# Kernel tuning notes

Hardware: AMD Instinct MI355X
Metric: run time of the kernel (lower is better)

Reference implementation:

```python
import jax, jax.numpy as jnp
import numpy as np


def setup_inputs() -> dict:
    key = jax.random.key(0)
    ks = jax.random.split(key, 8)
    B, H, W, C = 4, 64, 64, 64
    d = C // 8
    x = jax.random.normal(ks[0], (B, H, W, C), dtype=jnp.float32)
    # 1x1 conv kernels (spectral-normalized in the original; here we use the
    # already-normalized weight matrices directly, scaled to unit-ish norm)
    Wf = jax.random.normal(ks[1], (C, d), dtype=jnp.float32) * (1.0 / np.sqrt(C))
    bf = jnp.zeros((d,), dtype=jnp.float32)
    Wg = jax.random.normal(ks[2], (C, d), dtype=jnp.float32) * (1.0 / np.sqrt(C))
    bg = jnp.zeros((d,), dtype=jnp.float32)
    Wh = jax.random.normal(ks[3], (C, C), dtype=jnp.float32) * (1.0 / np.sqrt(C))
    bh = jnp.zeros((C,), dtype=jnp.float32)
    gamma = jnp.float32(1.0)
    return {"x": x, "Wf": Wf, "bf": bf, "Wg": Wg, "bg": bg,
            "Wh": Wh, "bh": bh, "gamma": gamma}


def reference(x, Wf, bf, Wg, bg, Wh, bh, gamma):
    # x: [B, H, W, C] (NHWC, as Keras Conv2D default)
    B, H, W, C = x.shape
    N = H * W
    # 1x1 convs == per-pixel channel matmuls
    q = jnp.einsum('bhwc,cd->bhwd', x, Wf) + bf   # [B,H,W,C//8]
    k = jnp.einsum('bhwc,cd->bhwd', x, Wg) + bg   # [B,H,W,C//8]
    v = jnp.einsum('bhwc,cd->bhwd', x, Wh) + bh   # [B,H,W,C]
    q = q.reshape(B, N, -1)
    k = k.reshape(B, N, -1)
    v = v.reshape(B, N, C)
    # full non-causal attention (no 1/sqrt(d) scaling in the original)
    s = jnp.einsum('bnd,bmd->bnm', q, k)          # [B,N,N]
    s = jax.nn.softmax(s, axis=-1)
    o = jnp.einsum('bnm,bmc->bnc', s, v)          # [B,N,C]
    o = o.reshape(B, H, W, C)
    return gamma * o + x
```

## Files before the change

kernel.cpp:

```cpp
#include <hip/hip_runtime.h>
#include <hip/hip_bf16.h>

#define BATCH 4
#define NTOK 4096
#define CCH 64
#define KSPLIT 4
#define KPB (NTOK / KSPLIT)
#define NTILE (KPB / 64)

typedef short s16x8 __attribute__((ext_vector_type(8)));
typedef float f32x4 __attribute__((ext_vector_type(4)));

static __device__ __forceinline__ unsigned short f2bf(float f) {
    union { __hip_bfloat16 h; unsigned short u; } cv;
    cv.h = __float2bfloat16(f);
    return cv.u;
}
static __device__ __forceinline__ float bf2f(unsigned short u) {
    union { unsigned int u; float f; } c; c.u = ((unsigned)u) << 16;
    return c.f;
}
static __device__ __forceinline__ float bf_split(float f, unsigned short& h) {
    h = f2bf(f);
    return f - bf2f(h);
}
static __device__ __forceinline__ unsigned pack_trunc(float a, float b) {
    union { float f; unsigned u; } ca, cb; ca.f = a; cb.f = b;
    return (ca.u >> 16) | (cb.u & 0xFFFF0000u);
}

__global__ __launch_bounds__(256) void proj_kernel(
    const float* __restrict__ xg,
    const float* __restrict__ Wf, const float* __restrict__ bf_,
    const float* __restrict__ Wg, const float* __restrict__ bg,
    const float* __restrict__ Wh, const float* __restrict__ bh,
    unsigned short* __restrict__ Qp, unsigned short* __restrict__ Kp,
    unsigned short* __restrict__ vTg)
{
    __shared__ float xS[32 * 68];
    __shared__ float WfT[8 * 68];
    __shared__ float WgT[8 * 68];
    __shared__ unsigned short vtS[64 * 40];

    const int t = threadIdx.x;
    const int b = blockIdx.x >> 7;
    const int n0 = (blockIdx.x & 127) * 32;

    const float* xrow = xg + ((size_t)b * NTOK + n0) * CCH;
    for (int f = t; f < 512; f += 256) {
        int r = f >> 4, c4 = (f & 15) * 4;
        *(float4*)(xS + r * 68 + c4) = *(const float4*)(xrow + r * 64 + c4);
    }
    for (int e = t; e < 512; e += 256) {
        int ci = e >> 3, j = e & 7;
        WfT[j * 68 + ci] = Wf[e];
        WgT[j * 68 + ci] = Wg[e];
    }
    __syncthreads();

    const int w = t >> 6, lane = t & 63, ml = lane & 15, quad = lane >> 4;

    {
        s16x8 a0, a1;
        #pragma unroll
        for (int j = 0; j < 8; ++j) {
            a0[j] = (short)f2bf(Wh[(quad * 8 + j) * 64 + w * 16 + ml]);
            a1[j] = (short)f2bf(Wh[(32 + quad * 8 + j) * 64 + w * 16 + ml]);
        }
        #pragma unroll
        for (int nf = 0; nf < 2; ++nf) {
            int tok = nf * 16 + ml;
            float4 r0 = *(const float4*)(xS + tok * 68 + quad * 8);
            float4 r1 = *(const float4*)(xS + tok * 68 + quad * 8 + 4);
            float4 r2 = *(const float4*)(xS + tok * 68 + 32 + quad * 8);
            float4 r3 = *(const float4*)(xS + tok * 68 + 32 + quad * 8 + 4);
            s16x8 b0, b1;
            b0[0] = (short)f2bf(r0.x); b0[1] = (short)f2bf(r0.y);
            b0[2] = (short)f2bf(r0.z); b0[3] = (short)f2bf(r0.w);
            b0[4] = (short)f2bf(r1.x); b0[5] = (short)f2bf(r1.y);
            b0[6] = (short)f2bf(r1.z); b0[7] = (short)f2bf(r1.w);
            b1[0] = (short)f2bf(r2.x); b1[1] = (short)f2bf(r2.y);
            b1[2] = (short)f2bf(r2.z); b1[3] = (short)f2bf(r2.w);
            b1[4] = (short)f2bf(r3.x); b1[5] = (short)f2bf(r3.y);
            b1[6] = (short)f2bf(r3.z); b1[7] = (short)f2bf(r3.w);
            f32x4 cc = __builtin_amdgcn_mfma_f32_16x16x32_bf16(a0, b0, (f32x4){0.f,0.f,0.f,0.f}, 0, 0, 0);
            cc = __builtin_amdgcn_mfma_f32_16x16x32_bf16(a1, b1, cc, 0, 0, 0);
            #pragma unroll
            for (int reg = 0; reg < 4; ++reg) {
                int cout = w * 16 + quad * 4 + reg;
                vtS[cout * 40 + nf * 16 + ml] = f2bf(cc[reg] + bh[cout]);
            }
        }
    }

    {
        int r = t >> 3, j = t & 7;
        float q = bf_[j], k = bg[j];
        for (int ci = 0; ci < 64; ci += 4) {
            float4 x4 = *(const float4*)(xS + r * 68 + ci);
            float4 wf4 = *(const float4*)(WfT + j * 68 + ci);
            float4 wg4 = *(const float4*)(WgT + j * 68 + ci);
            q += x4.x * wf4.x + x4.y * wf4.y + x4.z * wf4.z + x4.w * wf4.w;
            k += x4.x * wg4.x + x4.y * wg4.y + x4.z * wg4.z + x4.w * wg4.w;
        }
        unsigned short qh, kh;
        float qres = bf_split(q, qh);
        float kres = bf_split(k, kh);
        unsigned short ql = f2bf(qres), kl = f2bf(kres);
        size_t base = ((size_t)b * NTOK + n0 + r) * 32;
        Qp[base + j]      = qh;
        Qp[base + 8 + j]  = ql;
        Qp[base + 16 + j] = qh;
        Qp[base + 24 + j] = 0;
        Kp[base + j]      = kh;
        Kp[base + 8 + j]  = kh;
        Kp[base + 16 + j] = kl;
        Kp[base + 24 + j] = 0;
    }
    __syncthreads();

    {
        int c_ = t >> 2, chunk = t & 3;
        uint4 v = *(const uint4*)(vtS + c_ * 40 + chunk * 8);
        *(uint4*)(vTg + ((size_t)b * CCH + c_) * NTOK + n0 + chunk * 8) = v;
    }
}

__global__ __launch_bounds__(256, 4) void attn_kernel(
    const unsigned short* __restrict__ Qp,
    const unsigned short* __restrict__ Kp,
    const unsigned short* __restrict__ vTg,
    unsigned short* __restrict__ Opart,
    float* __restrict__ lpart)
{
    __shared__ unsigned short PS[2][64 * 72];

    const int t = threadIdx.x;
    const int blk = blockIdx.x;
    const int b = blk >> 8;
    const int qt = (blk >> 2) & 63;
    const int ks = blk & 3;
    const int m0 = qt * 64;
    const int kb0 = ks * KPB;
    const int w = t >> 6, lane = t & 63;
    const int ml = lane & 15, quad = lane >> 4;

    const unsigned short* qpb = Qp + (size_t)b * NTOK * 32;
    const unsigned short* kpb = Kp + (size_t)b * NTOK * 32;
    const unsigned short* vtb = vTg + (size_t)b * CCH * NTOK;

    s16x8 qf[4];
    #pragma unroll
    for (int g = 0; g < 4; ++g)
        qf[g] = *(const s16x8*)(qpb + (size_t)(m0 + g * 16 + ml) * 32 + quad * 8);

    s16x8 ones;
    #pragma unroll
    for (int i = 0; i < 8; ++i) ones[i] = (short)0x3F80;

    f32x4 o[4], l[4];
    #pragma unroll
    for (int g = 0; g < 4; ++g) { o[g] = (f32x4){0.f,0.f,0.f,0.f}; l[g] = (f32x4){0.f,0.f,0.f,0.f}; }
    const f32x4 zz = {0.f, 0.f, 0.f, 0.f};

    s16x8 kf = *(const s16x8*)(kpb + (size_t)(kb0 + w * 16 + ml) * 32 + quad * 8);

    for (int jt = 0; jt < NTILE; ++jt) {
        const int buf = jt & 1;
        const int kb = kb0 + jt * 64;

        f32x4 sg[4];
        #pragma unroll
        for (int g = 0; g < 4; ++g)
            sg[g] = __builtin_amdgcn_mfma_f32_16x16x32_bf16(kf, qf[g], zz, 0, 0, 0);

        {
            int kbn = kb0 + ((jt + 1) & (NTILE - 1)) * 64;
            kf = *(const s16x8*)(kpb + (size_t)(kbn + w * 16 + ml) * 32 + quad * 8);
        }
        s16x8 vf0 = *(const s16x8*)(vtb + (size_t)(w * 16 + ml) * NTOK + kb + quad * 8);
        s16x8 vf1 = *(const s16x8*)(vtb + (size_t)(w * 16 + ml) * NTOK + kb + 32 + quad * 8);

        #pragma unroll
        for (int g = 0; g < 4; ++g) {
            float p0 = exp2f(fmaf(sg[g][0], 1.442695041f, -28.85390082f));
            float p1 = exp2f(fmaf(sg[g][1], 1.442695041f, -28.85390082f));
            float p2 = exp2f(fmaf(sg[g][2], 1.442695041f, -28.85390082f));
            float p3 = exp2f(fmaf(sg[g][3], 1.442695041f, -28.85390082f));
            uint2 d = { pack_trunc(p0, p1), pack_trunc(p2, p3) };
            *(uint2*)(&PS[buf][(g * 16 + ml) * 72 + w * 16 + quad * 4]) = d;
        }
        __syncthreads();

        #pragma unroll
        for (int g = 0; g < 4; ++g) {
            s16x8 ap0 = *(const s16x8*)(&PS[buf][(g * 16 + ml) * 72 + quad * 8]);
            s16x8 ap1 = *(const s16x8*)(&PS[buf][(g * 16 + ml) * 72 + 32 + quad * 8]);
            l[g] = __builtin_amdgcn_mfma_f32_16x16x32_bf16(ap0, ones, l[g], 0, 0, 0);
            l[g] = __builtin_amdgcn_mfma_f32_16x16x32_bf16(ap1, ones, l[g], 0, 0, 0);
            o[g] = __builtin_amdgcn_mfma_f32_16x16x32_bf16(ap0, vf0, o[g], 0, 0, 0);
            o[g] = __builtin_amdgcn_mfma_f32_16x16x32_bf16(ap1, vf1, o[g], 0, 0, 0);
        }
    }

    const size_t obase = (size_t)ks * (BATCH * NTOK * 64)
                       + (size_t)b * NTOK * 64;
    #pragma unroll
    for (int g = 0; g < 4; ++g)
        #pragma unroll
        for (int reg = 0; reg < 4; ++reg) {
            int q = m0 + g * 16 + quad * 4 + reg;
            Opart[obase + (size_t)q * 64 + w * 16 + ml] = f2bf(o[g][reg]);
        }
    if (w == 0 && ml == 0) {
        #pragma unroll
        for (int g = 0; g < 4; ++g)
            #pragma unroll
            for (int reg = 0; reg < 4; ++reg)
                lpart[ks * (BATCH * NTOK) + b * NTOK + m0 + g * 16 + quad * 4 + reg] = l[g][reg];
    }
}

__global__ __launch_bounds__(256) void combine_kernel(
    const float* __restrict__ xg,
    const unsigned short* __restrict__ Opart,
    const float* __restrict__ lpart,
    const float* __restrict__ gammaPtr,
    float* __restrict__ out)
{
    const int i4 = blockIdx.x * 256 + threadIdx.x;
    const int base = i4 * 4;
    const int tok = base >> 6;

    float lsum = 0.f;
    #pragma unroll
    for (int s = 0; s < KSPLIT; ++s)
        lsum += lpart[s * (BATCH * NTOK) + tok];

    float o0 = 0.f, o1 = 0.f, o2 = 0.f, o3 = 0.f;
    #pragma unroll
    for (int s = 0; s < KSPLIT; ++s) {
        uint2 u = *(const uint2*)(Opart + (size_t)s * (BATCH * NTOK * 64) + base);
        o0 += bf2f((unsigned short)(u.x & 0xFFFF));
        o1 += bf2f((unsigned short)(u.x >> 16));
        o2 += bf2f((unsigned short)(u.y & 0xFFFF));
        o3 += bf2f((unsigned short)(u.y >> 16));
    }
    const float4 x4 = *(const float4*)(xg + base);
    const float gi = gammaPtr[0] / lsum;
    float4 r;
    r.x = gi * o0 + x4.x;
    r.y = gi * o1 + x4.y;
    r.z = gi * o2 + x4.z;
    r.w = gi * o3 + x4.w;
    *(float4*)(out + base) = r;
}

extern "C" void kernel_launch(void* const* d_in, const int* in_sizes, int n_in,
                              void* d_out, int out_size, void* d_ws, size_t ws_size,
                              hipStream_t stream) {
    const float* x  = (const float*)d_in[0];
    const float* Wf = (const float*)d_in[1];
    const float* bf = (const float*)d_in[2];
    const float* Wg = (const float*)d_in[3];
    const float* bg = (const float*)d_in[4];
    const float* Wh = (const float*)d_in[5];
    const float* bh = (const float*)d_in[6];
    const float* gamma = (const float*)d_in[7];
    float* out = (float*)d_out;

    char* ws = (char*)d_ws;
    unsigned short* Qp    = (unsigned short*)ws;
    unsigned short* Kp    = (unsigned short*)(ws + (1u << 20));
    unsigned short* vTg   = (unsigned short*)(ws + (2u << 20));
    unsigned short* Opart = (unsigned short*)(ws + (4u << 20));
    float*          lpart = (float*)(ws + (12u << 20));

    proj_kernel<<<BATCH * 128, 256, 0, stream>>>(x, Wf, bf, Wg, bg, Wh, bh,
                                                 Qp, Kp, vTg);
    attn_kernel<<<BATCH * 64 * KSPLIT, 256, 0, stream>>>(Qp, Kp, vTg, Opart, lpart);
    combine_kernel<<<(BATCH * NTOK * CCH) / 1024, 256, 0, stream>>>(x, Opart, lpart, gamma, out);
}
```

Measured before the change: 109.3 us.

## Keep P in registers, stage K/V tiles in LDS, coalesce output writes

Restructures the attention loop so each wave owns 16 query rows and computes S transposed (keys×queries). The exponentiated P then feeds the PV MFMA directly as the B operand, with no round trip through shared memory. K and V tiles are cooperatively loaded into double-buffered LDS, with global prefetch of the next tile overlapped with the exp work. The output is transposed through LDS for vectorized coalesced stores. This removes the per-tile P write/read and the redundant per-wave global V loads. In exchange it adds LDS traffic for K/V and a key-index permutation that must match the MFMA layout.

```diff
diff --git a/kernel.cpp b/kernel.cpp
--- a/kernel.cpp
+++ b/kernel.cpp
@@ -27,6 +27,9 @@
 static __device__ __forceinline__ unsigned pack_trunc(float a, float b) {
     union { float f; unsigned u; } ca, cb; ca.f = a; cb.f = b;
     return (ca.u >> 16) | (cb.u & 0xFFFF0000u);
+}
+static __device__ __forceinline__ unsigned pack_rne(float a, float b) {
+    return ((unsigned)f2bf(b) << 16) | f2bf(a);
 }
 
 __global__ __launch_bounds__(256) void proj_kernel(
@@ -133,7 +136,8 @@
     unsigned short* __restrict__ Opart,
     float* __restrict__ lpart)
 {
-    __shared__ unsigned short PS[2][64 * 72];
+    __shared__ unsigned short VS[2][64 * 72];
+    __shared__ unsigned short KS[2][64 * 36];
 
     const int t = threadIdx.x;
     const int blk = blockIdx.x;
@@ -149,75 +153,111 @@
     const unsigned short* kpb = Kp + (size_t)b * NTOK * 32;
     const unsigned short* vtb = vTg + (size_t)b * CCH * NTOK;
 
-    s16x8 qf[4];
-    #pragma unroll
-    for (int g = 0; g < 4; ++g)
-        qf[g] = *(const s16x8*)(qpb + (size_t)(m0 + g * 16 + ml) * 32 + quad * 8);
+    const s16x8 qf = *(const s16x8*)(qpb + (size_t)(m0 + w * 16 + ml) * 32 + quad * 8);
+
+    const int keyA = 8 * (ml >> 2) + (ml & 3);
 
     s16x8 ones;
     #pragma unroll
     for (int i = 0; i < 8; ++i) ones[i] = (short)0x3F80;
 
-    f32x4 o[4], l[4];
-    #pragma unroll
-    for (int g = 0; g < 4; ++g) { o[g] = (f32x4){0.f,0.f,0.f,0.f}; l[g] = (f32x4){0.f,0.f,0.f,0.f}; }
+    f32x4 o[4];
+    #pragma unroll
+    for (int cg = 0; cg < 4; ++cg) o[cg] = (f32x4){0.f, 0.f, 0.f, 0.f};
+    f32x4 lac = {0.f, 0.f, 0.f, 0.f};
     const f32x4 zz = {0.f, 0.f, 0.f, 0.f};
 
-    s16x8 kf = *(const s16x8*)(kpb + (size_t)(kb0 + w * 16 + ml) * 32 + quad * 8);
+    const int vrow = t >> 2, vcb = (t & 3) * 2;
+    const int krow = t >> 2, kpart = t & 3;
+
+    {
+        uint4 va = *(const uint4*)(vtb + (size_t)vrow * NTOK + kb0 + vcb * 8);
+        uint4 vb = *(const uint4*)(vtb + (size_t)vrow * NTOK + kb0 + (vcb + 1) * 8);
+        uint4 kk = *(const uint4*)(kpb + (size_t)(kb0 + krow) * 32 + kpart * 8);
+        *(uint4*)(&VS[0][vrow * 72 + vcb * 8]) = va;
+        *(uint4*)(&VS[0][vrow * 72 + (vcb + 1) * 8]) = vb;
+        *(uint4*)(&KS[0][krow * 36 + kpart * 8]) = kk;
+    }
 
     for (int jt = 0; jt < NTILE; ++jt) {
         const int buf = jt & 1;
-        const int kb = kb0 + jt * 64;
-
-        f32x4 sg[4];
+        __syncthreads();
+
+        const unsigned short* ksb = &KS[buf][0];
+        s16x8 kf0 = *(const s16x8*)(ksb + (keyA) * 36 + quad * 8);
+        s16x8 kf1 = *(const s16x8*)(ksb + (keyA + 4) * 36 + quad * 8);
+        s16x8 kf2 = *(const s16x8*)(ksb + (32 + keyA) * 36 + quad * 8);
+        s16x8 kf3 = *(const s16x8*)(ksb + (32 + keyA + 4) * 36 + quad * 8);
+
+        f32x4 sA0 = __builtin_amdgcn_mfma_f32_16x16x32_bf16(kf0, qf, zz, 0, 0, 0);
+        f32x4 sB0 = __builtin_amdgcn_mfma_f32_16x16x32_bf16(kf1, qf, zz, 0, 0, 0);
+        f32x4 sA1 = __builtin_amdgcn_mfma_f32_16x16x32_bf16(kf2, qf, zz, 0, 0, 0);
+        f32x4 sB1 = __builtin_amdgcn_mfma_f32_16x16x32_bf16(kf3, qf, zz, 0, 0, 0);
+
+        uint4 va, vb, kk;
+        const bool more = (jt + 1 < NTILE);
+        if (more) {
+            const int kbn = kb0 + (jt + 1) * 64;
+            va = *(const uint4*)(vtb + (size_t)vrow * NTOK + kbn + vcb * 8);
+            vb = *(const uint4*)(vtb + (size_t)vrow * NTOK + kbn + (vcb + 1) * 8);
+            kk = *(const uint4*)(kpb + (size_t)(kbn + krow) * 32 + kpart * 8);
+        }
+
+        union { unsigned u[4]; s16x8 h; } bf0, bf1;
+        bf0.u[0] = pack_trunc(exp2f(fmaf(sA0[0], 1.442695041f, -28.85390082f)),
+                              exp2f(fmaf(sA0[1], 1.442695041f, -28.85390082f)));
+        bf0.u[1] = pack_trunc(exp2f(fmaf(sA0[2], 1.442695041f, -28.85390082f)),
+                              exp2f(fmaf(sA0[3], 1.442695041f, -28.85390082f)));
+        bf0.u[2] = pack_trunc(exp2f(fmaf(sB0[0], 1.442695041f, -28.85390082f)),
+                              exp2f(fmaf(sB0[1], 1.442695041f, -28.85390082f)));
+        bf0.u[3] = pack_trunc(exp2f(fmaf(sB0[2], 1.442695041f, -28.85390082f)),
+                              exp2f(fmaf(sB0[3], 1.442695041f, -28.85390082f)));
+        bf1.u[0] = pack_trunc(exp2f(fmaf(sA1[0], 1.442695041f, -28.85390082f)),
+                              exp2f(fmaf(sA1[1], 1.442695041f, -28.85390082f)));
+        bf1.u[1] = pack_trunc(exp2f(fmaf(sA1[2], 1.442695041f, -28.85390082f)),
+                              exp2f(fmaf(sA1[3], 1.442695041f, -28.85390082f)));
+        bf1.u[2] = pack_trunc(exp2f(fmaf(sB1[0], 1.442695041f, -28.85390082f)),
+                              exp2f(fmaf(sB1[1], 1.442695041f, -28.85390082f)));
+        bf1.u[3] = pack_trunc(exp2f(fmaf(sB1[2], 1.442695041f, -28.85390082f)),
+                              exp2f(fmaf(sB1[3], 1.442695041f, -28.85390082f)));
+
+        if (more) {
+            *(uint4*)(&VS[buf ^ 1][vrow * 72 + vcb * 8]) = va;
+            *(uint4*)(&VS[buf ^ 1][vrow * 72 + (vcb + 1) * 8]) = vb;
+            *(uint4*)(&KS[buf ^ 1][krow * 36 + kpart * 8]) = kk;
+        }
+
+        lac = __builtin_amdgcn_mfma_f32_16x16x32_bf16(ones, bf0.h, lac, 0, 0, 0);
+        lac = __builtin_amdgcn_mfma_f32_16x16x32_bf16(ones, bf1.h, lac, 0, 0, 0);
+
+        const unsigned short* vs = &VS[buf][0];
         #pragma unroll
-        for (int g = 0; g < 4; ++g)
-            sg[g] = __builtin_amdgcn_mfma_f32_16x16x32_bf16(kf, qf[g], zz, 0, 0, 0);
-
-        {
-            int kbn = kb0 + ((jt + 1) & (NTILE - 1)) * 64;
-            kf = *(const s16x8*)(kpb + (size_t)(kbn + w * 16 + ml) * 32 + quad * 8);
-        }
-        s16x8 vf0 = *(const s16x8*)(vtb + (size_t)(w * 16 + ml) * NTOK + kb + quad * 8);
-        s16x8 vf1 = *(const s16x8*)(vtb + (size_t)(w * 16 + ml) * NTOK + kb + 32 + quad * 8);
-
-        #pragma unroll
-        for (int g = 0; g < 4; ++g) {
-            float p0 = exp2f(fmaf(sg[g][0], 1.442695041f, -28.85390082f));
-            float p1 = exp2f(fmaf(sg[g][1], 1.442695041f, -28.85390082f));
-            float p2 = exp2f(fmaf(sg[g][2], 1.442695041f, -28.85390082f));
-            float p3 = exp2f(fmaf(sg[g][3], 1.442695041f, -28.85390082f));
-            uint2 d = { pack_trunc(p0, p1), pack_trunc(p2, p3) };
-            *(uint2*)(&PS[buf][(g * 16 + ml) * 72 + w * 16 + quad * 4]) = d;
-        }
-        __syncthreads();
-
-        #pragma unroll
-        for (int g = 0; g < 4; ++g) {
-            s16x8 ap0 = *(const s16x8*)(&PS[buf][(g * 16 + ml) * 72 + quad * 8]);
-            s16x8 ap1 = *(const s16x8*)(&PS[buf][(g * 16 + ml) * 72 + 32 + quad * 8]);
-            l[g] = __builtin_amdgcn_mfma_f32_16x16x32_bf16(ap0, ones, l[g], 0, 0, 0);
-            l[g] = __builtin_amdgcn_mfma_f32_16x16x32_bf16(ap1, ones, l[g], 0, 0, 0);
-            o[g] = __builtin_amdgcn_mfma_f32_16x16x32_bf16(ap0, vf0, o[g], 0, 0, 0);
-            o[g] = __builtin_amdgcn_mfma_f32_16x16x32_bf16(ap1, vf1, o[g], 0, 0, 0);
-        }
-    }
-
-    const size_t obase = (size_t)ks * (BATCH * NTOK * 64)
-                       + (size_t)b * NTOK * 64;
-    #pragma unroll
-    for (int g = 0; g < 4; ++g)
-        #pragma unroll
-        for (int reg = 0; reg < 4; ++reg) {
-            int q = m0 + g * 16 + quad * 4 + reg;
-            Opart[obase + (size_t)q * 64 + w * 16 + ml] = f2bf(o[g][reg]);
-        }
-    if (w == 0 && ml == 0) {
-        #pragma unroll
-        for (int g = 0; g < 4; ++g)
-            #pragma unroll
-            for (int reg = 0; reg < 4; ++reg)
-                lpart[ks * (BATCH * NTOK) + b * NTOK + m0 + g * 16 + quad * 4 + reg] = l[g][reg];
+        for (int cg = 0; cg < 4; ++cg) {
+            s16x8 vA0 = *(const s16x8*)(vs + (cg * 16 + ml) * 72 + quad * 8);
+            s16x8 vA1 = *(const s16x8*)(vs + (cg * 16 + ml) * 72 + 32 + quad * 8);
+            o[cg] = __builtin_amdgcn_mfma_f32_16x16x32_bf16(vA0, bf0.h, o[cg], 0, 0, 0);
+            o[cg] = __builtin_amdgcn_mfma_f32_16x16x32_bf16(vA1, bf1.h, o[cg], 0, 0, 0);
+        }
+    }
+
+    if (quad == 0)
+        lpart[ks * (BATCH * NTOK) + b * NTOK + m0 + w * 16 + ml] = lac[0];
+
+    __syncthreads();
+    unsigned short* TR = &VS[0][0];
+    #pragma unroll
+    for (int cg = 0; cg < 4; ++cg) {
+        uint2 dd = { pack_rne(o[cg][0], o[cg][1]), pack_rne(o[cg][2], o[cg][3]) };
+        *(uint2*)(&TR[(w * 16 + ml) * 72 + cg * 16 + quad * 4]) = dd;
+    }
+    __syncthreads();
+    {
+        int ql = t >> 2, ch = t & 3;
+        uint4 u0 = *(const uint4*)(&TR[ql * 72 + ch * 16]);
+        uint4 u1 = *(const uint4*)(&TR[ql * 72 + ch * 16 + 8]);
+        size_t obase = ((size_t)ks * (BATCH * NTOK) + (size_t)b * NTOK + m0 + ql) * 64;
+        *(uint4*)(Opart + obase + ch * 16) = u0;
+        *(uint4*)(Opart + obase + ch * 16 + 8) = u1;
     }
 }
 
```

Measured after the change: 126.0 us. 15.3% more time.

## Restructure attention so each wave owns key tiles with register-resident P

Applied to the files above, without the earlier changes.

The attention kernel drops the shared-memory P exchange and the per-tile block barrier. Each wave now processes its own subset of key tiles for all 64 queries and all 64 channels, keeping P in registers as the MFMA B operand. Per-wave partial outputs and row sums are reduced through LDS at the end. The key split drops from 4 to 2, K is compacted to 16 halves and staged once in LDS, and proj_kernel converts x to bf16 once in shared memory. In exchange the kernel holds many more accumulator registers (occupancy bound lowered to 2 blocks per SIMD), runs fewer blocks, and adds a serialized end-of-kernel reduction.

```diff
diff --git a/kernel.cpp b/kernel.cpp
--- a/kernel.cpp
+++ b/kernel.cpp
@@ -4,12 +4,16 @@
 #define BATCH 4
 #define NTOK 4096
 #define CCH 64
-#define KSPLIT 4
+#define KSPLIT 2
 #define KPB (NTOK / KSPLIT)
 #define NTILE (KPB / 64)
+#define TPW (NTILE / 4)
 
 typedef short s16x8 __attribute__((ext_vector_type(8)));
 typedef float f32x4 __attribute__((ext_vector_type(4)));
+
+#define LOG2E 1.442695041f
+#define ESHIFT (-28.85390082f)
 
 static __device__ __forceinline__ unsigned short f2bf(float f) {
     union { __hip_bfloat16 h; unsigned short u; } cv;
@@ -27,6 +31,12 @@
 static __device__ __forceinline__ unsigned pack_trunc(float a, float b) {
     union { float f; unsigned u; } ca, cb; ca.f = a; cb.f = b;
     return (ca.u >> 16) | (cb.u & 0xFFFF0000u);
+}
+static __device__ __forceinline__ unsigned pack_rne(float a, float b) {
+    return ((unsigned)f2bf(b) << 16) | f2bf(a);
+}
+static __device__ __forceinline__ float pexp(float s) {
+    return exp2f(fmaf(s, LOG2E, ESHIFT));
 }
 
 __global__ __launch_bounds__(256) void proj_kernel(
@@ -38,6 +48,7 @@
     unsigned short* __restrict__ vTg)
 {
     __shared__ float xS[32 * 68];
+    __shared__ unsigned short xbS[32 * 72];
     __shared__ float WfT[8 * 68];
     __shared__ float WgT[8 * 68];
     __shared__ unsigned short vtS[64 * 40];
@@ -49,7 +60,10 @@
     const float* xrow = xg + ((size_t)b * NTOK + n0) * CCH;
     for (int f = t; f < 512; f += 256) {
         int r = f >> 4, c4 = (f & 15) * 4;
-        *(float4*)(xS + r * 68 + c4) = *(const float4*)(xrow + r * 64 + c4);
+        float4 v = *(const float4*)(xrow + r * 64 + c4);
+        *(float4*)(xS + r * 68 + c4) = v;
+        uint2 pk = { pack_rne(v.x, v.y), pack_rne(v.z, v.w) };
+        *(uint2*)(xbS + r * 72 + c4) = pk;
     }
     for (int e = t; e < 512; e += 256) {
         int ci = e >> 3, j = e & 7;
@@ -70,19 +84,8 @@
         #pragma unroll
         for (int nf = 0; nf < 2; ++nf) {
             int tok = nf * 16 + ml;
-            float4 r0 = *(const float4*)(xS + tok * 68 + quad * 8);
-            float4 r1 = *(const float4*)(xS + tok * 68 + quad * 8 + 4);
-            float4 r2 = *(const float4*)(xS + tok * 68 + 32 + quad * 8);
-            float4 r3 = *(const float4*)(xS + tok * 68 + 32 + quad * 8 + 4);
-            s16x8 b0, b1;
-            b0[0] = (short)f2bf(r0.x); b0[1] = (short)f2bf(r0.y);
-            b0[2] = (short)f2bf(r0.z); b0[3] = (short)f2bf(r0.w);
-            b0[4] = (short)f2bf(r1.x); b0[5] = (short)f2bf(r1.y);
-            b0[6] = (short)f2bf(r1.z); b0[7] = (short)f2bf(r1.w);
-            b1[0] = (short)f2bf(r2.x); b1[1] = (short)f2bf(r2.y);
-            b1[2] = (short)f2bf(r2.z); b1[3] = (short)f2bf(r2.w);
-            b1[4] = (short)f2bf(r3.x); b1[5] = (short)f2bf(r3.y);
-            b1[6] = (short)f2bf(r3.z); b1[7] = (short)f2bf(r3.w);
+            s16x8 b0 = *(const s16x8*)(xbS + tok * 72 + quad * 8);
+            s16x8 b1 = *(const s16x8*)(xbS + tok * 72 + 32 + quad * 8);
             f32x4 cc = __builtin_amdgcn_mfma_f32_16x16x32_bf16(a0, b0, (f32x4){0.f,0.f,0.f,0.f}, 0, 0, 0);
             cc = __builtin_amdgcn_mfma_f32_16x16x32_bf16(a1, b1, cc, 0, 0, 0);
             #pragma unroll
@@ -107,15 +110,14 @@
         float qres = bf_split(q, qh);
         float kres = bf_split(k, kh);
         unsigned short ql = f2bf(qres), kl = f2bf(kres);
-        size_t base = ((size_t)b * NTOK + n0 + r) * 32;
-        Qp[base + j]      = qh;
-        Qp[base + 8 + j]  = ql;
-        Qp[base + 16 + j] = qh;
-        Qp[base + 24 + j] = 0;
-        Kp[base + j]      = kh;
-        Kp[base + 8 + j]  = kh;
-        Kp[base + 16 + j] = kl;
-        Kp[base + 24 + j] = 0;
+        size_t qbase = ((size_t)b * NTOK + n0 + r) * 32;
+        Qp[qbase + j]      = qh;
+        Qp[qbase + 8 + j]  = ql;
+        Qp[qbase + 16 + j] = qh;
+        Qp[qbase + 24 + j] = 0;
+        size_t kbase = ((size_t)b * NTOK + n0 + r) * 16;
+        Kp[kbase + j]     = kh;
+        Kp[kbase + 8 + j] = kl;
     }
     __syncthreads();
 
@@ -126,99 +128,154 @@
     }
 }
 
-__global__ __launch_bounds__(256, 4) void attn_kernel(
+__global__ __launch_bounds__(256, 2) void attn_kernel(
     const unsigned short* __restrict__ Qp,
     const unsigned short* __restrict__ Kp,
     const unsigned short* __restrict__ vTg,
     unsigned short* __restrict__ Opart,
     float* __restrict__ lpart)
 {
-    __shared__ unsigned short PS[2][64 * 72];
+    __shared__ unsigned short KC[KPB * 16];
 
     const int t = threadIdx.x;
     const int blk = blockIdx.x;
-    const int b = blk >> 8;
-    const int qt = (blk >> 2) & 63;
-    const int ks = blk & 3;
+    const int b = blk >> 7;
+    const int qt = (blk >> 1) & 63;
+    const int ks = blk & 1;
     const int m0 = qt * 64;
     const int kb0 = ks * KPB;
     const int w = t >> 6, lane = t & 63;
     const int ml = lane & 15, quad = lane >> 4;
 
     const unsigned short* qpb = Qp + (size_t)b * NTOK * 32;
-    const unsigned short* kpb = Kp + (size_t)b * NTOK * 32;
+    const unsigned short* kpb = Kp + (size_t)b * NTOK * 16;
     const unsigned short* vtb = vTg + (size_t)b * CCH * NTOK;
 
+    for (int kk = t; kk < KPB; kk += 256) {
+        const unsigned short* src = kpb + (size_t)(kb0 + kk) * 16;
+        *(uint4*)(&KC[kk * 16])     = *(const uint4*)(src);
+        *(uint4*)(&KC[kk * 16 + 8]) = *(const uint4*)(src + 8);
+    }
+
     s16x8 qf[4];
     #pragma unroll
-    for (int g = 0; g < 4; ++g)
-        qf[g] = *(const s16x8*)(qpb + (size_t)(m0 + g * 16 + ml) * 32 + quad * 8);
-
+    for (int qg = 0; qg < 4; ++qg)
+        qf[qg] = *(const s16x8*)(qpb + (size_t)(m0 + qg * 16 + ml) * 32 + quad * 8);
+
+    const int keyA = 8 * (ml >> 2) + (ml & 3);
+    const int khsel = (quad == 2) ? 8 : 0;
     s16x8 ones;
     #pragma unroll
     for (int i = 0; i < 8; ++i) ones[i] = (short)0x3F80;
 
-    f32x4 o[4], l[4];
-    #pragma unroll
-    for (int g = 0; g < 4; ++g) { o[g] = (f32x4){0.f,0.f,0.f,0.f}; l[g] = (f32x4){0.f,0.f,0.f,0.f}; }
+    f32x4 o[4][4];
+    f32x4 lac[4];
+    #pragma unroll
+    for (int cg = 0; cg < 4; ++cg)
+        #pragma unroll
+        for (int qg = 0; qg < 4; ++qg) o[cg][qg] = (f32x4){0.f,0.f,0.f,0.f};
+    #pragma unroll
+    for (int qg = 0; qg < 4; ++qg) lac[qg] = (f32x4){0.f,0.f,0.f,0.f};
     const f32x4 zz = {0.f, 0.f, 0.f, 0.f};
 
-    s16x8 kf = *(const s16x8*)(kpb + (size_t)(kb0 + w * 16 + ml) * 32 + quad * 8);
-
-    for (int jt = 0; jt < NTILE; ++jt) {
-        const int buf = jt & 1;
-        const int kb = kb0 + jt * 64;
-
-        f32x4 sg[4];
-        #pragma unroll
-        for (int g = 0; g < 4; ++g)
-            sg[g] = __builtin_amdgcn_mfma_f32_16x16x32_bf16(kf, qf[g], zz, 0, 0, 0);
-
-        {
-            int kbn = kb0 + ((jt + 1) & (NTILE - 1)) * 64;
-            kf = *(const s16x8*)(kpb + (size_t)(kbn + w * 16 + ml) * 32 + quad * 8);
-        }
-        s16x8 vf0 = *(const s16x8*)(vtb + (size_t)(w * 16 + ml) * NTOK + kb + quad * 8);
-        s16x8 vf1 = *(const s16x8*)(vtb + (size_t)(w * 16 + ml) * NTOK + kb + 32 + quad * 8);
-
-        #pragma unroll
-        for (int g = 0; g < 4; ++g) {
-            float p0 = exp2f(fmaf(sg[g][0], 1.442695041f, -28.85390082f));
-            float p1 = exp2f(fmaf(sg[g][1], 1.442695041f, -28.85390082f));
-            float p2 = exp2f(fmaf(sg[g][2], 1.442695041f, -28.85390082f));
-            float p3 = exp2f(fmaf(sg[g][3], 1.442695041f, -28.85390082f));
-            uint2 d = { pack_trunc(p0, p1), pack_trunc(p2, p3) };
-            *(uint2*)(&PS[buf][(g * 16 + ml) * 72 + w * 16 + quad * 4]) = d;
-        }
+    __syncthreads();
+
+    const int tile0 = w * TPW;
+    s16x8 kf0 = *(const s16x8*)(&KC[(tile0 * 64 + keyA) * 16 + khsel]);
+    s16x8 kf1 = *(const s16x8*)(&KC[(tile0 * 64 + keyA + 4) * 16 + khsel]);
+    s16x8 kf2 = *(const s16x8*)(&KC[(tile0 * 64 + 32 + keyA) * 16 + khsel]);
+    s16x8 kf3 = *(const s16x8*)(&KC[(tile0 * 64 + 36 + keyA) * 16 + khsel]);
+
+    for (int i = 0; i < TPW; ++i) {
+        const int tile = w * TPW + i;
+        const int kb = kb0 + tile * 64;
+
+        s16x8 vf[4][2];
+        #pragma unroll
+        for (int cg = 0; cg < 4; ++cg) {
+            const unsigned short* vr = vtb + (size_t)(cg * 16 + ml) * NTOK + kb + quad * 8;
+            vf[cg][0] = *(const s16x8*)(vr);
+            vf[cg][1] = *(const s16x8*)(vr + 32);
+        }
+        const int tn = (i + 1 < TPW) ? tile + 1 : tile0;
+        s16x8 kn0 = *(const s16x8*)(&KC[(tn * 64 + keyA) * 16 + khsel]);
+        s16x8 kn1 = *(const s16x8*)(&KC[(tn * 64 + keyA + 4) * 16 + khsel]);
+        s16x8 kn2 = *(const s16x8*)(&KC[(tn * 64 + 32 + keyA) * 16 + khsel]);
+        s16x8 kn3 = *(const s16x8*)(&KC[(tn * 64 + 36 + keyA) * 16 + khsel]);
+
+        union { unsigned u[4]; s16x8 h; } P0[4], P1[4];
+        #pragma unroll
+        for (int qg = 0; qg < 4; ++qg) {
+            f32x4 sA0 = __builtin_amdgcn_mfma_f32_16x16x32_bf16(kf0, qf[qg], zz, 0, 0, 0);
+            f32x4 sB0 = __builtin_amdgcn_mfma_f32_16x16x32_bf16(kf1, qf[qg], zz, 0, 0, 0);
+            f32x4 sA1 = __builtin_amdgcn_mfma_f32_16x16x32_bf16(kf2, qf[qg], zz, 0, 0, 0);
+            f32x4 sB1 = __builtin_amdgcn_mfma_f32_16x16x32_bf16(kf3, qf[qg], zz, 0, 0, 0);
+            P0[qg].u[0] = pack_trunc(pexp(sA0[0]), pexp(sA0[1]));
+            P0[qg].u[1] = pack_trunc(pexp(sA0[2]), pexp(sA0[3]));
+            P0[qg].u[2] = pack_trunc(pexp(sB0[0]), pexp(sB0[1]));
+            P0[qg].u[3] = pack_trunc(pexp(sB0[2]), pexp(sB0[3]));
+            P1[qg].u[0] = pack_trunc(pexp(sA1[0]), pexp(sA1[1]));
+            P1[qg].u[1] = pack_trunc(pexp(sA1[2]), pexp(sA1[3]));
+            P1[qg].u[2] = pack_trunc(pexp(sB1[0]), pexp(sB1[1]));
+            P1[qg].u[3] = pack_trunc(pexp(sB1[2]), pexp(sB1[3]));
+        }
+        kf0 = kn0; kf1 = kn1; kf2 = kn2; kf3 = kn3;
+
+        #pragma unroll
+        for (int qg = 0; qg < 4; ++qg) {
+            lac[qg] = __builtin_amdgcn_mfma_f32_16x16x32_bf16(ones, P0[qg].h, lac[qg], 0, 0, 0);
+            lac[qg] = __builtin_amdgcn_mfma_f32_16x16x32_bf16(ones, P1[qg].h, lac[qg], 0, 0, 0);
+        }
+        #pragma unroll
+        for (int cg = 0; cg < 4; ++cg)
+            #pragma unroll
+            for (int qg = 0; qg < 4; ++qg) {
+                o[cg][qg] = __builtin_amdgcn_mfma_f32_16x16x32_bf16(vf[cg][0], P0[qg].h, o[cg][qg], 0, 0, 0);
+                o[cg][qg] = __builtin_amdgcn_mfma_f32_16x16x32_bf16(vf[cg][1], P1[qg].h, o[cg][qg], 0, 0, 0);
+            }
+    }
+
+    float* OL = (float*)KC;
+    float* lL = OL + 64 * 68;
+    #pragma unroll
+    for (int r = 0; r < 4; ++r) {
         __syncthreads();
-
-        #pragma unroll
-        for (int g = 0; g < 4; ++g) {
-            s16x8 ap0 = *(const s16x8*)(&PS[buf][(g * 16 + ml) * 72 + quad * 8]);
-            s16x8 ap1 = *(const s16x8*)(&PS[buf][(g * 16 + ml) * 72 + 32 + quad * 8]);
-            l[g] = __builtin_amdgcn_mfma_f32_16x16x32_bf16(ap0, ones, l[g], 0, 0, 0);
-            l[g] = __builtin_amdgcn_mfma_f32_16x16x32_bf16(ap1, ones, l[g], 0, 0, 0);
-            o[g] = __builtin_amdgcn_mfma_f32_16x16x32_bf16(ap0, vf0, o[g], 0, 0, 0);
-            o[g] = __builtin_amdgcn_mfma_f32_16x16x32_bf16(ap1, vf1, o[g], 0, 0, 0);
-        }
-    }
-
-    const size_t obase = (size_t)ks * (BATCH * NTOK * 64)
-                       + (size_t)b * NTOK * 64;
-    #pragma unroll
-    for (int g = 0; g < 4; ++g)
-        #pragma unroll
-        for (int reg = 0; reg < 4; ++reg) {
-            int q = m0 + g * 16 + quad * 4 + reg;
-            Opart[obase + (size_t)q * 64 + w * 16 + ml] = f2bf(o[g][reg]);
-        }
-    if (w == 0 && ml == 0) {
-        #pragma unroll
-        for (int g = 0; g < 4; ++g)
+        if (w == r) {
             #pragma unroll
-            for (int reg = 0; reg < 4; ++reg)
-                lpart[ks * (BATCH * NTOK) + b * NTOK + m0 + g * 16 + quad * 4 + reg] = l[g][reg];
-    }
+            for (int cg = 0; cg < 4; ++cg)
+                #pragma unroll
+                for (int qg = 0; qg < 4; ++qg) {
+                    f32x4* p = (f32x4*)(&OL[(qg * 16 + ml) * 68 + cg * 16 + quad * 4]);
+                    if (r == 0) *p = o[cg][qg];
+                    else {
+                        f32x4 v = *p;
+                        v[0] += o[cg][qg][0]; v[1] += o[cg][qg][1];
+                        v[2] += o[cg][qg][2]; v[3] += o[cg][qg][3];
+                        *p = v;
+                    }
+                }
+            if (quad == 0) {
+                #pragma unroll
+                for (int qg = 0; qg < 4; ++qg) {
+                    if (r == 0) lL[qg * 16 + ml] = lac[qg][0];
+                    else        lL[qg * 16 + ml] += lac[qg][0];
+                }
+            }
+        }
+    }
+    __syncthreads();
+
+    {
+        int q = t >> 2, c0 = (t & 3) * 16;
+        alignas(16) unsigned short us[16];
+        #pragma unroll
+        for (int k = 0; k < 16; ++k) us[k] = f2bf(OL[q * 68 + c0 + k]);
+        size_t obase = ((size_t)ks * (BATCH * NTOK) + (size_t)b * NTOK + m0 + q) * 64 + c0;
+        *(uint4*)(Opart + obase)     = *(uint4*)(us);
+        *(uint4*)(Opart + obase + 8) = *(uint4*)(us + 8);
+    }
+    if (t < 64)
+        lpart[ks * (BATCH * NTOK) + b * NTOK + m0 + t] = lL[t];
 }
 
 __global__ __launch_bounds__(256) void combine_kernel(
@@ -274,7 +331,7 @@
     unsigned short* Kp    = (unsigned short*)(ws + (1u << 20));
     unsigned short* vTg   = (unsigned short*)(ws + (2u << 20));
     unsigned short* Opart = (unsigned short*)(ws + (4u << 20));
-    float*          lpart = (float*)(ws + (12u << 20));
+    float*          lpart = (float*)(ws + (8u << 20));
 
     proj_kernel<<<BATCH * 128, 256, 0, stream>>>(x, Wf, bf, Wg, bg, Wh, bh,
                                                  Qp, Kp, vTg);
```

Result: no change. 111.1 us (+1.6%).
